# Kernel tuning notes

Hardware: AMD Instinct MI355X
Metric: run time of the kernel (lower is better)

The kernel has to match this reference:

```python
import jax, jax.numpy as jnp
import numpy as np

F_IN, F_OUT, H, L_ENC, L_DEC, HORIZON = 32, 8, 64, 2, 2, 48
B, T = 2048, 512


def _lstm_cell(x, h, c, Wih, Whh, bih, bhh):
    # PyTorch LSTMCell: gates ordered i, f, g, o
    g = x @ Wih.T + bih + h @ Whh.T + bhh
    i, f, gg, o = jnp.split(g, 4, axis=-1)
    c_new = jax.nn.sigmoid(f) * c + jax.nn.sigmoid(i) * jnp.tanh(gg)
    h_new = jax.nn.sigmoid(o) * jnp.tanh(c_new)
    return h_new, c_new


def setup_inputs() -> dict:
    key = jax.random.key(0)
    ks = jax.random.split(key, 16)
    s = 1.0 / np.sqrt(H)
    u = lambda k, shape: jax.random.uniform(k, shape, jnp.float32, -s, s)
    return {
        "X": jax.random.normal(ks[0], (B, T, F_IN), jnp.float32),
        "X_mask": jnp.ones((B, T, F_IN), jnp.float32),
        "W_emb": u(ks[1], (H, F_IN)),
        "b_emb": u(ks[2], (H,)),
        "enc_Wih": u(ks[3], (L_ENC, 4 * H, H)),
        "enc_Whh": u(ks[4], (L_ENC, 4 * H, H)),
        "enc_bih": u(ks[5], (L_ENC, 4 * H)),
        "enc_bhh": u(ks[6], (L_ENC, 4 * H)),
        "dec_Wih": u(ks[7], (L_DEC, 4 * H, H)),
        "dec_Whh": u(ks[8], (L_DEC, 4 * H, H)),
        "dec_bih": u(ks[9], (L_DEC, 4 * H)),
        "dec_bhh": u(ks[10], (L_DEC, 4 * H)),
        "W_reg": u(ks[11], (F_OUT, H)),
        "b_reg": u(ks[12], (F_OUT,)),
    }


def reference(X, X_mask, W_emb, b_emb, enc_Wih, enc_Whh, enc_bih, enc_bhh,
              dec_Wih, dec_Whh, dec_bih, dec_bhh, W_reg, b_reg):
    batch = X.shape[0]
    # Token embedding for all timesteps at once: [T, B, H]
    emb = jnp.einsum('btf,hf->tbh', X, W_emb) + b_emb

    h0 = jnp.zeros((L_ENC, batch, H), X.dtype)
    c0 = jnp.zeros((L_ENC, batch, H), X.dtype)

    def enc_step(carry, x_t):
        h, c = carry
        h_t = x_t
        hs, cs = [], []
        for i in range(L_ENC):
            h_t, c_t = _lstm_cell(h_t, h[i], c[i], enc_Wih[i], enc_Whh[i], enc_bih[i], enc_bhh[i])
            hs.append(h_t)
            cs.append(c_t)
        return (jnp.stack(hs), jnp.stack(cs)), None

    (h_enc, _), _ = jax.lax.scan(enc_step, (h0, c0), emb)

    # Decoder: hidden states initialized from encoder h, cells from zero
    c_dec0 = jnp.zeros((L_DEC, batch, H), X.dtype)

    def dec_step(carry, _):
        h, c = carry
        h_t = h[-1]
        hs, cs = [], []
        for i in range(L_DEC):
            h_t, c_t = _lstm_cell(h_t, h[i], c[i], dec_Wih[i], dec_Whh[i], dec_bih[i], dec_bhh[i])
            hs.append(h_t)
            cs.append(c_t)
        y_t = h_t @ W_reg.T + b_reg
        return (jnp.stack(hs), jnp.stack(cs)), y_t

    _, ys = jax.lax.scan(dec_step, (h_enc, c_dec0), None, length=HORIZON)
    return jnp.transpose(ys, (1, 0, 2))  # [B, horizon, F_OUT]
```

## Files before the change

kernel.cpp:

```cpp
#include <hip/hip_runtime.h>
#include <hip/hip_bf16.h>

typedef __bf16 bf16x8 __attribute__((ext_vector_type(8)));
typedef float  f32x4  __attribute__((ext_vector_type(4)));

#define MFMA16(a,b,c) __builtin_amdgcn_mfma_f32_16x16x32_bf16((a),(b),(c),0,0,0)

__device__ __forceinline__ bf16x8 cvt8(f32x4 a, f32x4 b){
  bf16x8 r;
  r[0]=(__bf16)a[0]; r[1]=(__bf16)a[1]; r[2]=(__bf16)a[2]; r[3]=(__bf16)a[3];
  r[4]=(__bf16)b[0]; r[5]=(__bf16)b[1]; r[6]=(__bf16)b[2]; r[7]=(__bf16)b[3];
  return r;
}
__device__ __forceinline__ bf16x8 ld8(const float* p){
  return cvt8(*(const f32x4*)p, *(const f32x4*)(p+4));
}
__device__ __forceinline__ float sigm(float x){
  return __builtin_amdgcn_rcpf(1.f + __expf(-x));
}
__device__ __forceinline__ float tanhx(float x){
  return 1.f - 2.f*__builtin_amdgcn_rcpf(1.f + __expf(2.f*x));
}
__device__ __forceinline__ f32x4 sp(float v){ return (f32x4){v,v,v,v}; }

extern "C" __global__ void __launch_bounds__(512, 1)
seq2seq_kernel(const float* __restrict__ X,
               const float* __restrict__ Wemb, const float* __restrict__ bemb,
               const float* __restrict__ eWih, const float* __restrict__ eWhh,
               const float* __restrict__ ebih, const float* __restrict__ ebhh,
               const float* __restrict__ dWih, const float* __restrict__ dWhh,
               const float* __restrict__ dbih, const float* __restrict__ dbhh,
               const float* __restrict__ Wreg, const float* __restrict__ breg,
               float* __restrict__ out)
{
  __shared__ __align__(16) __bf16 XA[2][8][136];
  __shared__ __align__(16) __bf16 H1s[8][72];
  __shared__ __align__(16) float  Gm[2][8][260];

  const int tid  = (int)threadIdx.x;
  const int w    = tid >> 6;
  const int grp  = w >> 2;
  const bool g0  = (grp == 0);
  const int wt   = w & 3;
  const int lane = tid & 63;
  const int col  = lane & 15;
  const int quad = lane >> 4;
  const int row8 = col & 7;
  const int b0   = (int)blockIdx.x * 8;
  const int brow = b0 + row8;

  for (int i = tid; i < 2*8*136; i += 512) (&XA[0][0][0])[i] = (__bf16)0.f;
  for (int i = tid; i < 8*72;    i += 512) (&H1s[0][0])[i]   = (__bf16)0.f;

  const int ue = wt*16 + col;
  bf16x8 wembf = ld8(Wemb + ue*32 + quad*8);
  const float eb = bemb[ue];

  bf16x8 wr[2];
#pragma unroll
  for (int ks=0; ks<2; ++ks) wr[ks] = ld8(Wreg + (col&7)*64 + ks*32 + quad*8);
  const float rb = breg[col&7];

  bf16x8 wf[16];
  float  gb[4];
#pragma unroll
  for (int j=0; j<4; ++j){
    const int n = 64*wt + 16*j + col;
    gb[j] = ebih[grp*256+n] + ebhh[grp*256+n];
#pragma unroll
    for (int ks=0; ks<4; ++ks){
      const float* srcw = (ks < 2) ? eWih : eWhh;
      wf[j*4+ks] = ld8(srcw + ((size_t)(grp*256+n))*64 + (ks&1)*32 + quad*8);
    }
  }

  float cA = 0.f, cB = 0.f;
  const float* xb = X + (size_t)brow*512*32 + quad*8;
  f32x4 pa0, pb0, pa1, pb1;
  f32x4 x0a = *(const f32x4*)xb, x0b = *(const f32x4*)(xb+4);
  pa1 = *(const f32x4*)(xb+32); pb1 = *(const f32x4*)(xb+36);
  pa0 = *(const f32x4*)(xb+64); pb0 = *(const f32x4*)(xb+68);

  auto GEMM0 = [&](const int I){
    const int Px = (I+1)&1, Pr = I&1;
    bf16x8 ax0 = *(const bf16x8*)&XA[Px][row8][ 0 + quad*8];
    bf16x8 ax1 = *(const bf16x8*)&XA[Px][row8][32 + quad*8];
    bf16x8 ah0 = *(const bf16x8*)&XA[Pr][row8][64 + quad*8];
    bf16x8 ah1 = *(const bf16x8*)&XA[Pr][row8][96 + quad*8];
    f32x4 A0=sp(gb[0]), A1=sp(gb[1]), A2=sp(gb[2]), A3=sp(gb[3]);
    A0=MFMA16(ax0,wf[0],A0);  A1=MFMA16(ax0,wf[4],A1);
    A2=MFMA16(ax0,wf[8],A2);  A3=MFMA16(ax0,wf[12],A3);
    A0=MFMA16(ax1,wf[1],A0);  A1=MFMA16(ax1,wf[5],A1);
    A2=MFMA16(ax1,wf[9],A2);  A3=MFMA16(ax1,wf[13],A3);
    A0=MFMA16(ah0,wf[2],A0);  A1=MFMA16(ah0,wf[6],A1);
    A2=MFMA16(ah0,wf[10],A2); A3=MFMA16(ah0,wf[14],A3);
    A0=MFMA16(ah1,wf[3],A0);  A1=MFMA16(ah1,wf[7],A1);
    A2=MFMA16(ah1,wf[11],A2); A3=MFMA16(ah1,wf[15],A3);
    if (I < 510){
      const int s = I&1;
      f32x4 xr0 = s ? pa1 : pa0, xr1 = s ? pb1 : pb0;
      f32x4 ea = MFMA16(cvt8(xr0,xr1), wembf, sp(eb));
      int tn = I+4; if (tn > 511) tn = 511;
      f32x4 na = *(const f32x4*)(xb + (size_t)tn*32);
      f32x4 nb = *(const f32x4*)(xb + (size_t)tn*32 + 4);
      if (s){ pa1=na; pb1=nb; } else { pa0=na; pb0=nb; }
      if (quad < 2){
#pragma unroll
        for (int r=0; r<4; ++r) XA[s][quad*4+r][ue] = (__bf16)ea[r];
      }
    }
    f32x4 t0 = (quad&2) ? A2 : A0;
    f32x4 t1 = (quad&2) ? A3 : A1;
    const int rb2 = (quad&1)*4;
    const int nn  = 64*wt + ((quad&2)?32:0) + col;
#pragma unroll
    for (int r=0; r<4; ++r){ Gm[0][rb2+r][nn] = t0[r]; Gm[0][rb2+r][nn+16] = t1[r]; }
  };

  auto GEMM1 = [&](const int I){
    const int Pr = I&1;
    bf16x8 ah0 = *(const bf16x8*)&XA[Pr][row8][64 + quad*8];
    bf16x8 ah1 = *(const bf16x8*)&XA[Pr][row8][96 + quad*8];
    bf16x8 ag0 = *(const bf16x8*)&H1s[row8][quad*8];
    bf16x8 ag1 = *(const bf16x8*)&H1s[row8][32 + quad*8];
    f32x4 A0=sp(gb[0]), A1=sp(gb[1]), A2=sp(gb[2]), A3=sp(gb[3]);
    A0=MFMA16(ah0,wf[0],A0);  A1=MFMA16(ah0,wf[4],A1);
    A2=MFMA16(ah0,wf[8],A2);  A3=MFMA16(ah0,wf[12],A3);
    A0=MFMA16(ah1,wf[1],A0);  A1=MFMA16(ah1,wf[5],A1);
    A2=MFMA16(ah1,wf[9],A2);  A3=MFMA16(ah1,wf[13],A3);
    A0=MFMA16(ag0,wf[2],A0);  A1=MFMA16(ag0,wf[6],A1);
    A2=MFMA16(ag0,wf[10],A2); A3=MFMA16(ag0,wf[14],A3);
    A0=MFMA16(ag1,wf[3],A0);  A1=MFMA16(ag1,wf[7],A1);
    A2=MFMA16(ag1,wf[11],A2); A3=MFMA16(ag1,wf[15],A3);
    f32x4 t0 = (quad&2) ? A2 : A0;
    f32x4 t1 = (quad&2) ? A3 : A1;
    const int rb2 = (quad&1)*4;
    const int nn  = 64*wt + ((quad&2)?32:0) + col;
#pragma unroll
    for (int r=0; r<4; ++r){ Gm[1][rb2+r][nn] = t0[r]; Gm[1][rb2+r][nn+16] = t1[r]; }
  };

  auto EW0 = [&](const int I){
    const int Pw = (I+1)&1;
    const float* ga = Gm[0][wt];
    const float* gc = Gm[0][wt+4];
    float iA=sigm(ga[lane]),    iB=sigm(gc[lane]);
    float fA=sigm(ga[64+lane]), fB=sigm(gc[64+lane]);
    float gA=tanhx(ga[128+lane]), gB=tanhx(gc[128+lane]);
    float oA=sigm(ga[192+lane]),  oB=sigm(gc[192+lane]);
    cA = fA*cA + iA*gA;
    cB = fB*cB + iB*gB;
    XA[Pw][wt  ][64+lane] = (__bf16)(oA*tanhx(cA));
    XA[Pw][wt+4][64+lane] = (__bf16)(oB*tanhx(cB));
  };

  auto EW1 = [&](){
    const float* ga = Gm[1][wt];
    const float* gc = Gm[1][wt+4];
    float iA=sigm(ga[lane]),    iB=sigm(gc[lane]);
    float fA=sigm(ga[64+lane]), fB=sigm(gc[64+lane]);
    float gA=tanhx(ga[128+lane]), gB=tanhx(gc[128+lane]);
    float oA=sigm(ga[192+lane]),  oB=sigm(gc[192+lane]);
    cA = fA*cA + iA*gA;
    cB = fB*cB + iB*gB;
    H1s[wt  ][lane] = (__bf16)(oA*tanhx(cA));
    H1s[wt+4][lane] = (__bf16)(oB*tanhx(cB));
  };

  __syncthreads();

  if (g0){
    f32x4 e0 = MFMA16(cvt8(x0a,x0b), wembf, sp(eb));
    if (quad < 2){
#pragma unroll
      for (int r=0; r<4; ++r) XA[0][quad*4+r][ue] = (__bf16)e0[r];
    }
  }
  __syncthreads();
  if (g0) GEMM0(-1);
  __syncthreads();
  if (g0) EW0(-1);
  __syncthreads();

#define SLOT(I)                                              \
  if (g0) GEMM0(I); else { if ((I) > 0) EW1(); }             \
  __syncthreads();                                           \
  if (g0) EW0(I); else GEMM1(I);                             \
  __syncthreads();

  for (int ii=0; ii<255; ++ii){
    SLOT(2*ii)
    SLOT(2*ii+1)
  }
  SLOT(510)
#undef SLOT

  if (!g0) EW1();
  __syncthreads();
  if (!g0) GEMM1(511);
  __syncthreads();
  if (!g0) EW1();
  __syncthreads();

  for (int idx = tid; idx < 8*128; idx += 512){
    int r = idx >> 7, cc = idx & 127;
    XA[0][r][cc] = (cc < 64) ? H1s[r][cc] : XA[1][r][cc];
  }
#pragma unroll
  for (int l=0; l<2; ++l)
#pragma unroll
    for (int ti=0; ti<2; ++ti){
      const int n = 32*w + 16*ti + col;
      gb[l*2+ti] = dbih[l*256+n] + dbhh[l*256+n];
#pragma unroll
      for (int ks=0; ks<4; ++ks){
        const float* srcw = (ks < 2) ? dWih : dWhh;
        wf[(l*2+ti)*4+ks] = ld8(srcw + ((size_t)(l*256+n))*64 + (ks&1)*32 + quad*8);
      }
    }
  float cD0 = 0.f, cD1 = 0.f;
  __syncthreads();

  auto Ystore = [&](const int t){
    f32x4 ya = sp(rb);
    bf16x8 y0 = *(const bf16x8*)&H1s[row8][quad*8];
    bf16x8 y1 = *(const bf16x8*)&H1s[row8][32 + quad*8];
    ya = MFMA16(y0, wr[0], ya);
    ya = MFMA16(y1, wr[1], ya);
    if (quad < 2 && col < 8){
#pragma unroll
      for (int r=0; r<4; ++r)
        out[((size_t)(b0 + quad*4 + r)*48 + t)*8 + col] = ya[r];
    }
  };

  for (int t=0; t<48; ++t){
    {
      bf16x8 ax0 = *(const bf16x8*)&XA[0][row8][ 0 + quad*8];
      bf16x8 ax1 = *(const bf16x8*)&XA[0][row8][32 + quad*8];
      bf16x8 ah0 = *(const bf16x8*)&XA[0][row8][64 + quad*8];
      bf16x8 ah1 = *(const bf16x8*)&XA[0][row8][96 + quad*8];
      f32x4 B0 = sp(gb[0]), B1 = sp(gb[1]);
      B0=MFMA16(ax0,wf[0],B0); B1=MFMA16(ax0,wf[4],B1);
      B0=MFMA16(ax1,wf[1],B0); B1=MFMA16(ax1,wf[5],B1);
      B0=MFMA16(ah0,wf[2],B0); B1=MFMA16(ah0,wf[6],B1);
      B0=MFMA16(ah1,wf[3],B0); B1=MFMA16(ah1,wf[7],B1);
      f32x4 t0 = (quad&2) ? B1 : B0;
      const int rb2 = (quad&1)*4, nn = 32*w + ((quad&2)?16:0) + col;
#pragma unroll
      for (int r=0; r<4; ++r) Gm[0][rb2+r][nn] = t0[r];
      if (t && w == 0) Ystore(t-1);
    }
    __syncthreads();
    {
      const float* g = Gm[0][w];
      float i0=sigm(g[lane]), f0=sigm(g[64+lane]);
      float gg=tanhx(g[128+lane]), o0=sigm(g[192+lane]);
      cD0 = f0*cD0 + i0*gg;
      XA[0][w][64+lane] = (__bf16)(o0*tanhx(cD0));
    }
    __syncthreads();
    {
      bf16x8 ah0 = *(const bf16x8*)&XA[0][row8][64 + quad*8];
      bf16x8 ah1 = *(const bf16x8*)&XA[0][row8][96 + quad*8];
      bf16x8 ag0 = *(const bf16x8*)&H1s[row8][quad*8];
      bf16x8 ag1 = *(const bf16x8*)&H1s[row8][32 + quad*8];
      f32x4 B0 = sp(gb[2]), B1 = sp(gb[3]);
      B0=MFMA16(ah0,wf[8],B0);  B1=MFMA16(ah0,wf[12],B1);
      B0=MFMA16(ah1,wf[9],B0);  B1=MFMA16(ah1,wf[13],B1);
      B0=MFMA16(ag0,wf[10],B0); B1=MFMA16(ag0,wf[14],B1);
      B0=MFMA16(ag1,wf[11],B0); B1=MFMA16(ag1,wf[15],B1);
      f32x4 t0 = (quad&2) ? B1 : B0;
      const int rb2 = (quad&1)*4, nn = 32*w + ((quad&2)?16:0) + col;
#pragma unroll
      for (int r=0; r<4; ++r) Gm[1][rb2+r][nn] = t0[r];
    }
    __syncthreads();
    {
      const float* g = Gm[1][w];
      float i1=sigm(g[lane]), f1=sigm(g[64+lane]);
      float gg=tanhx(g[128+lane]), o1=sigm(g[192+lane]);
      cD1 = f1*cD1 + i1*gg;
      __bf16 hb = (__bf16)(o1*tanhx(cD1));
      H1s[w][lane]  = hb;
      XA[0][w][lane] = hb;
    }
    __syncthreads();
  }
  if (w == 0) Ystore(47);
}

extern "C" void kernel_launch(void* const* d_in, const int* in_sizes, int n_in,
                              void* d_out, int out_size, void* d_ws, size_t ws_size,
                              hipStream_t stream)
{
  (void)in_sizes; (void)n_in; (void)out_size; (void)d_ws; (void)ws_size;
  const float* X    = (const float*)d_in[0];
  const float* Wemb = (const float*)d_in[2];
  const float* bemb = (const float*)d_in[3];
  const float* eWih = (const float*)d_in[4];
  const float* eWhh = (const float*)d_in[5];
  const float* ebih = (const float*)d_in[6];
  const float* ebhh = (const float*)d_in[7];
  const float* dWih = (const float*)d_in[8];
  const float* dWhh = (const float*)d_in[9];
  const float* dbih = (const float*)d_in[10];
  const float* dbhh = (const float*)d_in[11];
  const float* Wreg = (const float*)d_in[12];
  const float* breg = (const float*)d_in[13];
  float* out = (float*)d_out;

  seq2seq_kernel<<<dim3(256), dim3(512), 0, stream>>>(
      X, Wemb, bemb, eWih, eWhh, ebih, ebhh,
      dWih, dWhh, dbih, dbhh, Wreg, breg, out);
}
```

Before: 651.6 us.

## Double threads per block to split LSTM gate work across sixteen waves

Raises the block from 512 to 1024 threads, so each layer group has eight waves instead of four. Each wave now computes two gate tiles instead of four and runs the elementwise update for one batch row instead of two. The decoder is remapped so that waves 0-7 and 8-15 each handle one layer's elementwise step. The goal is to shorten the per-step serial critical path inside the recurrence. In exchange, barriers now cover twice as many waves, and during the decoder's elementwise phases half the waves sit idle.

After: 628.4 us. 3.5% less time.

```diff
diff --git a/kernel.cpp b/kernel.cpp
--- a/kernel.cpp
+++ b/kernel.cpp
@@ -23,7 +23,7 @@
 }
 __device__ __forceinline__ f32x4 sp(float v){ return (f32x4){v,v,v,v}; }
 
-extern "C" __global__ void __launch_bounds__(512, 1)
+extern "C" __global__ void __launch_bounds__(1024, 4)
 seq2seq_kernel(const float* __restrict__ X,
                const float* __restrict__ Wemb, const float* __restrict__ bemb,
                const float* __restrict__ eWih, const float* __restrict__ eWhh,
@@ -33,15 +33,15 @@
                const float* __restrict__ Wreg, const float* __restrict__ breg,
                float* __restrict__ out)
 {
-  __shared__ __align__(16) __bf16 XA[2][8][136];
-  __shared__ __align__(16) __bf16 H1s[8][72];
-  __shared__ __align__(16) float  Gm[2][8][260];
+  __shared__ __align__(16) __bf16 XA[2][8][144];
+  __shared__ __align__(16) __bf16 H1s[8][80];
+  __shared__ __align__(16) float  Gm[2][8][264];
 
   const int tid  = (int)threadIdx.x;
   const int w    = tid >> 6;
-  const int grp  = w >> 2;
+  const int grp  = w >> 3;
   const bool g0  = (grp == 0);
-  const int wt   = w & 3;
+  const int wt   = w & 7;
   const int lane = tid & 63;
   const int col  = lane & 15;
   const int quad = lane >> 4;
@@ -49,37 +49,35 @@
   const int b0   = (int)blockIdx.x * 8;
   const int brow = b0 + row8;
 
-  for (int i = tid; i < 2*8*136; i += 512) (&XA[0][0][0])[i] = (__bf16)0.f;
-  for (int i = tid; i < 8*72;    i += 512) (&H1s[0][0])[i]   = (__bf16)0.f;
-
-  const int ue = wt*16 + col;
-  bf16x8 wembf = ld8(Wemb + ue*32 + quad*8);
-  const float eb = bemb[ue];
-
-  bf16x8 wr[2];
-#pragma unroll
-  for (int ks=0; ks<2; ++ks) wr[ks] = ld8(Wreg + (col&7)*64 + ks*32 + quad*8);
-  const float rb = breg[col&7];
-
-  bf16x8 wf[16];
-  float  gb[4];
-#pragma unroll
-  for (int j=0; j<4; ++j){
-    const int n = 64*wt + 16*j + col;
-    gb[j] = ebih[grp*256+n] + ebhh[grp*256+n];
+  for (int i = tid; i < 2*8*144; i += 1024) (&XA[0][0][0])[i] = (__bf16)0.f;
+  for (int i = tid; i < 8*80;    i += 1024) (&H1s[0][0])[i]   = (__bf16)0.f;
+
+  bf16x8 wf[8];
+  float  gb[2];
+#pragma unroll
+  for (int ti=0; ti<2; ++ti){
+    const int n = 32*wt + 16*ti + col;
+    gb[ti] = ebih[grp*256+n] + ebhh[grp*256+n];
 #pragma unroll
     for (int ks=0; ks<4; ++ks){
       const float* srcw = (ks < 2) ? eWih : eWhh;
-      wf[j*4+ks] = ld8(srcw + ((size_t)(grp*256+n))*64 + (ks&1)*32 + quad*8);
-    }
-  }
-
-  float cA = 0.f, cB = 0.f;
+      wf[ti*4+ks] = ld8(srcw + ((size_t)(grp*256+n))*64 + (ks&1)*32 + quad*8);
+    }
+  }
+
+  const int ue = (w&3)*16 + col;
+  bf16x8 wembf;
+  float eb = 0.f;
   const float* xb = X + (size_t)brow*512*32 + quad*8;
   f32x4 pa0, pb0, pa1, pb1;
-  f32x4 x0a = *(const f32x4*)xb, x0b = *(const f32x4*)(xb+4);
-  pa1 = *(const f32x4*)(xb+32); pb1 = *(const f32x4*)(xb+36);
-  pa0 = *(const f32x4*)(xb+64); pb0 = *(const f32x4*)(xb+68);
+  if (w < 4){
+    wembf = ld8(Wemb + ue*32 + quad*8);
+    eb = bemb[ue];
+    pa1 = *(const f32x4*)(xb+32); pb1 = *(const f32x4*)(xb+36);
+    pa0 = *(const f32x4*)(xb+64); pb0 = *(const f32x4*)(xb+68);
+  }
+
+  float cC = 0.f;
 
   auto GEMM0 = [&](const int I){
     const int Px = (I+1)&1, Pr = I&1;
@@ -87,16 +85,12 @@
     bf16x8 ax1 = *(const bf16x8*)&XA[Px][row8][32 + quad*8];
     bf16x8 ah0 = *(const bf16x8*)&XA[Pr][row8][64 + quad*8];
     bf16x8 ah1 = *(const bf16x8*)&XA[Pr][row8][96 + quad*8];
-    f32x4 A0=sp(gb[0]), A1=sp(gb[1]), A2=sp(gb[2]), A3=sp(gb[3]);
-    A0=MFMA16(ax0,wf[0],A0);  A1=MFMA16(ax0,wf[4],A1);
-    A2=MFMA16(ax0,wf[8],A2);  A3=MFMA16(ax0,wf[12],A3);
-    A0=MFMA16(ax1,wf[1],A0);  A1=MFMA16(ax1,wf[5],A1);
-    A2=MFMA16(ax1,wf[9],A2);  A3=MFMA16(ax1,wf[13],A3);
-    A0=MFMA16(ah0,wf[2],A0);  A1=MFMA16(ah0,wf[6],A1);
-    A2=MFMA16(ah0,wf[10],A2); A3=MFMA16(ah0,wf[14],A3);
-    A0=MFMA16(ah1,wf[3],A0);  A1=MFMA16(ah1,wf[7],A1);
-    A2=MFMA16(ah1,wf[11],A2); A3=MFMA16(ah1,wf[15],A3);
-    if (I < 510){
+    f32x4 A0 = sp(gb[0]), A1 = sp(gb[1]);
+    A0=MFMA16(ax0,wf[0],A0); A1=MFMA16(ax0,wf[4],A1);
+    A0=MFMA16(ax1,wf[1],A0); A1=MFMA16(ax1,wf[5],A1);
+    A0=MFMA16(ah0,wf[2],A0); A1=MFMA16(ah0,wf[6],A1);
+    A0=MFMA16(ah1,wf[3],A0); A1=MFMA16(ah1,wf[7],A1);
+    if (I < 510 && w < 4){
       const int s = I&1;
       f32x4 xr0 = s ? pa1 : pa0, xr1 = s ? pb1 : pb0;
       f32x4 ea = MFMA16(cvt8(xr0,xr1), wembf, sp(eb));
@@ -109,12 +103,11 @@
         for (int r=0; r<4; ++r) XA[s][quad*4+r][ue] = (__bf16)ea[r];
       }
     }
-    f32x4 t0 = (quad&2) ? A2 : A0;
-    f32x4 t1 = (quad&2) ? A3 : A1;
+    f32x4 t0 = (quad&2) ? A1 : A0;
     const int rb2 = (quad&1)*4;
-    const int nn  = 64*wt + ((quad&2)?32:0) + col;
-#pragma unroll
-    for (int r=0; r<4; ++r){ Gm[0][rb2+r][nn] = t0[r]; Gm[0][rb2+r][nn+16] = t1[r]; }
+    const int nn  = 32*wt + ((quad&2)?16:0) + col;
+#pragma unroll
+    for (int r=0; r<4; ++r) Gm[0][rb2+r][nn] = t0[r];
   };
 
   auto GEMM1 = [&](const int I){
@@ -123,53 +116,39 @@
     bf16x8 ah1 = *(const bf16x8*)&XA[Pr][row8][96 + quad*8];
     bf16x8 ag0 = *(const bf16x8*)&H1s[row8][quad*8];
     bf16x8 ag1 = *(const bf16x8*)&H1s[row8][32 + quad*8];
-    f32x4 A0=sp(gb[0]), A1=sp(gb[1]), A2=sp(gb[2]), A3=sp(gb[3]);
-    A0=MFMA16(ah0,wf[0],A0);  A1=MFMA16(ah0,wf[4],A1);
-    A2=MFMA16(ah0,wf[8],A2);  A3=MFMA16(ah0,wf[12],A3);
-    A0=MFMA16(ah1,wf[1],A0);  A1=MFMA16(ah1,wf[5],A1);
-    A2=MFMA16(ah1,wf[9],A2);  A3=MFMA16(ah1,wf[13],A3);
-    A0=MFMA16(ag0,wf[2],A0);  A1=MFMA16(ag0,wf[6],A1);
-    A2=MFMA16(ag0,wf[10],A2); A3=MFMA16(ag0,wf[14],A3);
-    A0=MFMA16(ag1,wf[3],A0);  A1=MFMA16(ag1,wf[7],A1);
-    A2=MFMA16(ag1,wf[11],A2); A3=MFMA16(ag1,wf[15],A3);
-    f32x4 t0 = (quad&2) ? A2 : A0;
-    f32x4 t1 = (quad&2) ? A3 : A1;
+    f32x4 A0 = sp(gb[0]), A1 = sp(gb[1]);
+    A0=MFMA16(ah0,wf[0],A0); A1=MFMA16(ah0,wf[4],A1);
+    A0=MFMA16(ah1,wf[1],A0); A1=MFMA16(ah1,wf[5],A1);
+    A0=MFMA16(ag0,wf[2],A0); A1=MFMA16(ag0,wf[6],A1);
+    A0=MFMA16(ag1,wf[3],A0); A1=MFMA16(ag1,wf[7],A1);
+    f32x4 t0 = (quad&2) ? A1 : A0;
     const int rb2 = (quad&1)*4;
-    const int nn  = 64*wt + ((quad&2)?32:0) + col;
-#pragma unroll
-    for (int r=0; r<4; ++r){ Gm[1][rb2+r][nn] = t0[r]; Gm[1][rb2+r][nn+16] = t1[r]; }
+    const int nn  = 32*wt + ((quad&2)?16:0) + col;
+#pragma unroll
+    for (int r=0; r<4; ++r) Gm[1][rb2+r][nn] = t0[r];
   };
 
   auto EW0 = [&](const int I){
     const int Pw = (I+1)&1;
-    const float* ga = Gm[0][wt];
-    const float* gc = Gm[0][wt+4];
-    float iA=sigm(ga[lane]),    iB=sigm(gc[lane]);
-    float fA=sigm(ga[64+lane]), fB=sigm(gc[64+lane]);
-    float gA=tanhx(ga[128+lane]), gB=tanhx(gc[128+lane]);
-    float oA=sigm(ga[192+lane]),  oB=sigm(gc[192+lane]);
-    cA = fA*cA + iA*gA;
-    cB = fB*cB + iB*gB;
-    XA[Pw][wt  ][64+lane] = (__bf16)(oA*tanhx(cA));
-    XA[Pw][wt+4][64+lane] = (__bf16)(oB*tanhx(cB));
+    const float* g = Gm[0][wt];
+    float i0=sigm(g[lane]),      f0=sigm(g[64+lane]);
+    float gg=tanhx(g[128+lane]), o0=sigm(g[192+lane]);
+    cC = f0*cC + i0*gg;
+    XA[Pw][wt][64+lane] = (__bf16)(o0*tanhx(cC));
   };
 
   auto EW1 = [&](){
-    const float* ga = Gm[1][wt];
-    const float* gc = Gm[1][wt+4];
-    float iA=sigm(ga[lane]),    iB=sigm(gc[lane]);
-    float fA=sigm(ga[64+lane]), fB=sigm(gc[64+lane]);
-    float gA=tanhx(ga[128+lane]), gB=tanhx(gc[128+lane]);
-    float oA=sigm(ga[192+lane]),  oB=sigm(gc[192+lane]);
-    cA = fA*cA + iA*gA;
-    cB = fB*cB + iB*gB;
-    H1s[wt  ][lane] = (__bf16)(oA*tanhx(cA));
-    H1s[wt+4][lane] = (__bf16)(oB*tanhx(cB));
-  };
-
-  __syncthreads();
-
-  if (g0){
+    const float* g = Gm[1][wt];
+    float i1=sigm(g[lane]),      f1=sigm(g[64+lane]);
+    float gg=tanhx(g[128+lane]), o1=sigm(g[192+lane]);
+    cC = f1*cC + i1*gg;
+    H1s[wt][lane] = (__bf16)(o1*tanhx(cC));
+  };
+
+  __syncthreads();
+
+  if (w < 4){
+    f32x4 x0a = *(const f32x4*)xb, x0b = *(const f32x4*)(xb+4);
     f32x4 e0 = MFMA16(cvt8(x0a,x0b), wembf, sp(eb));
     if (quad < 2){
 #pragma unroll
@@ -202,31 +181,33 @@
   if (!g0) EW1();
   __syncthreads();
 
-  for (int idx = tid; idx < 8*128; idx += 512){
+  for (int idx = tid; idx < 8*128; idx += 1024){
     int r = idx >> 7, cc = idx & 127;
     XA[0][r][cc] = (cc < 64) ? H1s[r][cc] : XA[1][r][cc];
   }
-#pragma unroll
-  for (int l=0; l<2; ++l)
-#pragma unroll
-    for (int ti=0; ti<2; ++ti){
-      const int n = 32*w + 16*ti + col;
-      gb[l*2+ti] = dbih[l*256+n] + dbhh[l*256+n];
-#pragma unroll
-      for (int ks=0; ks<4; ++ks){
-        const float* srcw = (ks < 2) ? dWih : dWhh;
-        wf[(l*2+ti)*4+ks] = ld8(srcw + ((size_t)(l*256+n))*64 + (ks&1)*32 + quad*8);
-      }
-    }
-  float cD0 = 0.f, cD1 = 0.f;
+  bf16x8 wr0 = ld8(Wreg + (col&7)*64 +  0 + quad*8);
+  bf16x8 wr1 = ld8(Wreg + (col&7)*64 + 32 + quad*8);
+  const float rb = breg[col&7];
+  float gbd[2];
+#pragma unroll
+  for (int l=0; l<2; ++l){
+    const int n = 16*w + col;
+    gbd[l] = dbih[l*256+n] + dbhh[l*256+n];
+#pragma unroll
+    for (int ks=0; ks<4; ++ks){
+      const float* srcw = (ks < 2) ? dWih : dWhh;
+      wf[l*4+ks] = ld8(srcw + ((size_t)(l*256+n))*64 + (ks&1)*32 + quad*8);
+    }
+  }
+  cC = 0.f;
   __syncthreads();
 
   auto Ystore = [&](const int t){
     f32x4 ya = sp(rb);
     bf16x8 y0 = *(const bf16x8*)&H1s[row8][quad*8];
     bf16x8 y1 = *(const bf16x8*)&H1s[row8][32 + quad*8];
-    ya = MFMA16(y0, wr[0], ya);
-    ya = MFMA16(y1, wr[1], ya);
+    ya = MFMA16(y0, wr0, ya);
+    ya = MFMA16(y1, wr1, ya);
     if (quad < 2 && col < 8){
 #pragma unroll
       for (int r=0; r<4; ++r)
@@ -240,24 +221,24 @@
       bf16x8 ax1 = *(const bf16x8*)&XA[0][row8][32 + quad*8];
       bf16x8 ah0 = *(const bf16x8*)&XA[0][row8][64 + quad*8];
       bf16x8 ah1 = *(const bf16x8*)&XA[0][row8][96 + quad*8];
-      f32x4 B0 = sp(gb[0]), B1 = sp(gb[1]);
-      B0=MFMA16(ax0,wf[0],B0); B1=MFMA16(ax0,wf[4],B1);
-      B0=MFMA16(ax1,wf[1],B0); B1=MFMA16(ax1,wf[5],B1);
-      B0=MFMA16(ah0,wf[2],B0); B1=MFMA16(ah0,wf[6],B1);
-      B0=MFMA16(ah1,wf[3],B0); B1=MFMA16(ah1,wf[7],B1);
-      f32x4 t0 = (quad&2) ? B1 : B0;
-      const int rb2 = (quad&1)*4, nn = 32*w + ((quad&2)?16:0) + col;
-#pragma unroll
-      for (int r=0; r<4; ++r) Gm[0][rb2+r][nn] = t0[r];
+      f32x4 B0 = sp(gbd[0]);
+      B0=MFMA16(ax0,wf[0],B0);
+      B0=MFMA16(ax1,wf[1],B0);
+      B0=MFMA16(ah0,wf[2],B0);
+      B0=MFMA16(ah1,wf[3],B0);
+      if (quad < 2){
+#pragma unroll
+        for (int r=0; r<4; ++r) Gm[0][quad*4+r][16*w+col] = B0[r];
+      }
       if (t && w == 0) Ystore(t-1);
     }
     __syncthreads();
-    {
+    if (w < 8){
       const float* g = Gm[0][w];
-      float i0=sigm(g[lane]), f0=sigm(g[64+lane]);
+      float i0=sigm(g[lane]),      f0=sigm(g[64+lane]);
       float gg=tanhx(g[128+lane]), o0=sigm(g[192+lane]);
-      cD0 = f0*cD0 + i0*gg;
-      XA[0][w][64+lane] = (__bf16)(o0*tanhx(cD0));
+      cC = f0*cC + i0*gg;
+      XA[0][w][64+lane] = (__bf16)(o0*tanhx(cC));
     }
     __syncthreads();
     {
@@ -265,25 +246,26 @@
       bf16x8 ah1 = *(const bf16x8*)&XA[0][row8][96 + quad*8];
       bf16x8 ag0 = *(const bf16x8*)&H1s[row8][quad*8];
       bf16x8 ag1 = *(const bf16x8*)&H1s[row8][32 + quad*8];
-      f32x4 B0 = sp(gb[2]), B1 = sp(gb[3]);
-      B0=MFMA16(ah0,wf[8],B0);  B1=MFMA16(ah0,wf[12],B1);
-      B0=MFMA16(ah1,wf[9],B0);  B1=MFMA16(ah1,wf[13],B1);
-      B0=MFMA16(ag0,wf[10],B0); B1=MFMA16(ag0,wf[14],B1);
-      B0=MFMA16(ag1,wf[11],B0); B1=MFMA16(ag1,wf[15],B1);
-      f32x4 t0 = (quad&2) ? B1 : B0;
-      const int rb2 = (quad&1)*4, nn = 32*w + ((quad&2)?16:0) + col;
-#pragma unroll
-      for (int r=0; r<4; ++r) Gm[1][rb2+r][nn] = t0[r];
-    }
-    __syncthreads();
-    {
-      const float* g = Gm[1][w];
-      float i1=sigm(g[lane]), f1=sigm(g[64+lane]);
+      f32x4 B1 = sp(gbd[1]);
+      B1=MFMA16(ah0,wf[4],B1);
+      B1=MFMA16(ah1,wf[5],B1);
+      B1=MFMA16(ag0,wf[6],B1);
+      B1=MFMA16(ag1,wf[7],B1);
+      if (quad < 2){
+#pragma unroll
+        for (int r=0; r<4; ++r) Gm[1][quad*4+r][16*w+col] = B1[r];
+      }
+    }
+    __syncthreads();
+    if (w >= 8){
+      const int rw = w - 8;
+      const float* g = Gm[1][rw];
+      float i1=sigm(g[lane]),      f1=sigm(g[64+lane]);
       float gg=tanhx(g[128+lane]), o1=sigm(g[192+lane]);
-      cD1 = f1*cD1 + i1*gg;
-      __bf16 hb = (__bf16)(o1*tanhx(cD1));
-      H1s[w][lane]  = hb;
-      XA[0][w][lane] = hb;
+      cC = f1*cC + i1*gg;
+      __bf16 hb = (__bf16)(o1*tanhx(cC));
+      H1s[rw][lane]   = hb;
+      XA[0][rw][lane] = hb;
     }
     __syncthreads();
   }
@@ -310,7 +292,7 @@
   const float* breg = (const float*)d_in[13];
   float* out = (float*)d_out;
 
-  seq2seq_kernel<<<dim3(256), dim3(512), 0, stream>>>(
+  seq2seq_kernel<<<dim3(256), dim3(1024), 0, stream>>>(
       X, Wemb, bemb, eWih, eWhh, ebih, ebhh,
       dWih, dWhh, dbih, dbhh, Wreg, breg, out);
 }
```

## Halve batch rows per block to launch twice as many blocks

Applied to the files above, without the earlier changes.

Each block now handles 4 batch rows instead of 8, and the grid doubles from 256 to 512 blocks. Launch bounds are relaxed to allow multiple blocks per CU. The elementwise and gate-store mappings are rearranged so each wave handles one row, and in the decoder the two layers' elementwise work is split between the wave halves. The aim is to fill more CUs, since the strictly serial time recurrence leaves the machine underused. The trade-off is that the 16-row MFMA tiles are now only a quarter used, so more matrix instructions are wasted per useful row.

New measurement: 1.660 ms. 155% more time.

```diff
diff --git a/kernel.cpp b/kernel.cpp
--- a/kernel.cpp
+++ b/kernel.cpp
@@ -23,7 +23,7 @@
 }
 __device__ __forceinline__ f32x4 sp(float v){ return (f32x4){v,v,v,v}; }
 
-extern "C" __global__ void __launch_bounds__(512, 1)
+extern "C" __global__ void __launch_bounds__(512, 4)
 seq2seq_kernel(const float* __restrict__ X,
                const float* __restrict__ Wemb, const float* __restrict__ bemb,
                const float* __restrict__ eWih, const float* __restrict__ eWhh,
@@ -33,33 +33,24 @@
                const float* __restrict__ Wreg, const float* __restrict__ breg,
                float* __restrict__ out)
 {
-  __shared__ __align__(16) __bf16 XA[2][8][136];
-  __shared__ __align__(16) __bf16 H1s[8][72];
-  __shared__ __align__(16) float  Gm[2][8][260];
+  __shared__ __align__(16) __bf16 XA[2][4][144];
+  __shared__ __align__(16) __bf16 H1s[4][80];
+  __shared__ __align__(16) float  Gm[2][4][264];
 
   const int tid  = (int)threadIdx.x;
   const int w    = tid >> 6;
+  const bool g0  = (w < 4);
   const int grp  = w >> 2;
-  const bool g0  = (grp == 0);
   const int wt   = w & 3;
   const int lane = tid & 63;
   const int col  = lane & 15;
   const int quad = lane >> 4;
-  const int row8 = col & 7;
-  const int b0   = (int)blockIdx.x * 8;
-  const int brow = b0 + row8;
-
-  for (int i = tid; i < 2*8*136; i += 512) (&XA[0][0][0])[i] = (__bf16)0.f;
-  for (int i = tid; i < 8*72;    i += 512) (&H1s[0][0])[i]   = (__bf16)0.f;
-
-  const int ue = wt*16 + col;
-  bf16x8 wembf = ld8(Wemb + ue*32 + quad*8);
-  const float eb = bemb[ue];
-
-  bf16x8 wr[2];
-#pragma unroll
-  for (int ks=0; ks<2; ++ks) wr[ks] = ld8(Wreg + (col&7)*64 + ks*32 + quad*8);
-  const float rb = breg[col&7];
+  const int row4 = col & 3;
+  const int b0   = (int)blockIdx.x * 4;
+  const int brow = b0 + row4;
+
+  for (int i = tid; i < 2*4*144; i += 512) (&XA[0][0][0])[i] = (__bf16)0.f;
+  for (int i = tid; i < 4*80;    i += 512) (&H1s[0][0])[i]   = (__bf16)0.f;
 
   bf16x8 wf[16];
   float  gb[4];
@@ -74,19 +65,26 @@
     }
   }
 
-  float cA = 0.f, cB = 0.f;
+  const int ue = wt*16 + col;
+  bf16x8 wembf;
+  float eb = 0.f;
   const float* xb = X + (size_t)brow*512*32 + quad*8;
   f32x4 pa0, pb0, pa1, pb1;
-  f32x4 x0a = *(const f32x4*)xb, x0b = *(const f32x4*)(xb+4);
-  pa1 = *(const f32x4*)(xb+32); pb1 = *(const f32x4*)(xb+36);
-  pa0 = *(const f32x4*)(xb+64); pb0 = *(const f32x4*)(xb+68);
+  if (g0){
+    wembf = ld8(Wemb + ue*32 + quad*8);
+    eb = bemb[ue];
+    pa1 = *(const f32x4*)(xb+32); pb1 = *(const f32x4*)(xb+36);
+    pa0 = *(const f32x4*)(xb+64); pb0 = *(const f32x4*)(xb+68);
+  }
+
+  float cC = 0.f;
 
   auto GEMM0 = [&](const int I){
     const int Px = (I+1)&1, Pr = I&1;
-    bf16x8 ax0 = *(const bf16x8*)&XA[Px][row8][ 0 + quad*8];
-    bf16x8 ax1 = *(const bf16x8*)&XA[Px][row8][32 + quad*8];
-    bf16x8 ah0 = *(const bf16x8*)&XA[Pr][row8][64 + quad*8];
-    bf16x8 ah1 = *(const bf16x8*)&XA[Pr][row8][96 + quad*8];
+    bf16x8 ax0 = *(const bf16x8*)&XA[Px][row4][ 0 + quad*8];
+    bf16x8 ax1 = *(const bf16x8*)&XA[Px][row4][32 + quad*8];
+    bf16x8 ah0 = *(const bf16x8*)&XA[Pr][row4][64 + quad*8];
+    bf16x8 ah1 = *(const bf16x8*)&XA[Pr][row4][96 + quad*8];
     f32x4 A0=sp(gb[0]), A1=sp(gb[1]), A2=sp(gb[2]), A3=sp(gb[3]);
     A0=MFMA16(ax0,wf[0],A0);  A1=MFMA16(ax0,wf[4],A1);
     A2=MFMA16(ax0,wf[8],A2);  A3=MFMA16(ax0,wf[12],A3);
@@ -104,25 +102,25 @@
       f32x4 na = *(const f32x4*)(xb + (size_t)tn*32);
       f32x4 nb = *(const f32x4*)(xb + (size_t)tn*32 + 4);
       if (s){ pa1=na; pb1=nb; } else { pa0=na; pb0=nb; }
-      if (quad < 2){
-#pragma unroll
-        for (int r=0; r<4; ++r) XA[s][quad*4+r][ue] = (__bf16)ea[r];
+      if (quad == 0){
+#pragma unroll
+        for (int r=0; r<4; ++r) XA[s][r][ue] = (__bf16)ea[r];
       }
     }
-    f32x4 t0 = (quad&2) ? A2 : A0;
-    f32x4 t1 = (quad&2) ? A3 : A1;
-    const int rb2 = (quad&1)*4;
-    const int nn  = 64*wt + ((quad&2)?32:0) + col;
-#pragma unroll
-    for (int r=0; r<4; ++r){ Gm[0][rb2+r][nn] = t0[r]; Gm[0][rb2+r][nn+16] = t1[r]; }
+    f32x4 u0 = (quad&1) ? A1 : A0;
+    f32x4 u1 = (quad&1) ? A3 : A2;
+    f32x4 t  = (quad&2) ? u1 : u0;
+    const int nn = 64*wt + 16*quad + col;
+#pragma unroll
+    for (int r=0; r<4; ++r) Gm[0][r][nn] = t[r];
   };
 
   auto GEMM1 = [&](const int I){
     const int Pr = I&1;
-    bf16x8 ah0 = *(const bf16x8*)&XA[Pr][row8][64 + quad*8];
-    bf16x8 ah1 = *(const bf16x8*)&XA[Pr][row8][96 + quad*8];
-    bf16x8 ag0 = *(const bf16x8*)&H1s[row8][quad*8];
-    bf16x8 ag1 = *(const bf16x8*)&H1s[row8][32 + quad*8];
+    bf16x8 ah0 = *(const bf16x8*)&XA[Pr][row4][64 + quad*8];
+    bf16x8 ah1 = *(const bf16x8*)&XA[Pr][row4][96 + quad*8];
+    bf16x8 ag0 = *(const bf16x8*)&H1s[row4][quad*8];
+    bf16x8 ag1 = *(const bf16x8*)&H1s[row4][32 + quad*8];
     f32x4 A0=sp(gb[0]), A1=sp(gb[1]), A2=sp(gb[2]), A3=sp(gb[3]);
     A0=MFMA16(ah0,wf[0],A0);  A1=MFMA16(ah0,wf[4],A1);
     A2=MFMA16(ah0,wf[8],A2);  A3=MFMA16(ah0,wf[12],A3);
@@ -132,48 +130,39 @@
     A2=MFMA16(ag0,wf[10],A2); A3=MFMA16(ag0,wf[14],A3);
     A0=MFMA16(ag1,wf[3],A0);  A1=MFMA16(ag1,wf[7],A1);
     A2=MFMA16(ag1,wf[11],A2); A3=MFMA16(ag1,wf[15],A3);
-    f32x4 t0 = (quad&2) ? A2 : A0;
-    f32x4 t1 = (quad&2) ? A3 : A1;
-    const int rb2 = (quad&1)*4;
-    const int nn  = 64*wt + ((quad&2)?32:0) + col;
-#pragma unroll
-    for (int r=0; r<4; ++r){ Gm[1][rb2+r][nn] = t0[r]; Gm[1][rb2+r][nn+16] = t1[r]; }
+    f32x4 u0 = (quad&1) ? A1 : A0;
+    f32x4 u1 = (quad&1) ? A3 : A2;
+    f32x4 t  = (quad&2) ? u1 : u0;
+    const int nn = 64*wt + 16*quad + col;
+#pragma unroll
+    for (int r=0; r<4; ++r) Gm[1][r][nn] = t[r];
   };
 
   auto EW0 = [&](const int I){
     const int Pw = (I+1)&1;
-    const float* ga = Gm[0][wt];
-    const float* gc = Gm[0][wt+4];
-    float iA=sigm(ga[lane]),    iB=sigm(gc[lane]);
-    float fA=sigm(ga[64+lane]), fB=sigm(gc[64+lane]);
-    float gA=tanhx(ga[128+lane]), gB=tanhx(gc[128+lane]);
-    float oA=sigm(ga[192+lane]),  oB=sigm(gc[192+lane]);
-    cA = fA*cA + iA*gA;
-    cB = fB*cB + iB*gB;
-    XA[Pw][wt  ][64+lane] = (__bf16)(oA*tanhx(cA));
-    XA[Pw][wt+4][64+lane] = (__bf16)(oB*tanhx(cB));
+    const float* g = Gm[0][wt];
+    float i0=sigm(g[lane]),      f0=sigm(g[64+lane]);
+    float gg=tanhx(g[128+lane]), o0=sigm(g[192+lane]);
+    cC = f0*cC + i0*gg;
+    XA[Pw][wt][64+lane] = (__bf16)(o0*tanhx(cC));
   };
 
   auto EW1 = [&](){
-    const float* ga = Gm[1][wt];
-    const float* gc = Gm[1][wt+4];
-    float iA=sigm(ga[lane]),    iB=sigm(gc[lane]);
-    float fA=sigm(ga[64+lane]), fB=sigm(gc[64+lane]);
-    float gA=tanhx(ga[128+lane]), gB=tanhx(gc[128+lane]);
-    float oA=sigm(ga[192+lane]),  oB=sigm(gc[192+lane]);
-    cA = fA*cA + iA*gA;
-    cB = fB*cB + iB*gB;
-    H1s[wt  ][lane] = (__bf16)(oA*tanhx(cA));
-    H1s[wt+4][lane] = (__bf16)(oB*tanhx(cB));
+    const float* g = Gm[1][wt];
+    float i1=sigm(g[lane]),      f1=sigm(g[64+lane]);
+    float gg=tanhx(g[128+lane]), o1=sigm(g[192+lane]);
+    cC = f1*cC + i1*gg;
+    H1s[wt][lane] = (__bf16)(o1*tanhx(cC));
   };
 
   __syncthreads();
 
   if (g0){
+    f32x4 x0a = *(const f32x4*)xb, x0b = *(const f32x4*)(xb+4);
     f32x4 e0 = MFMA16(cvt8(x0a,x0b), wembf, sp(eb));
-    if (quad < 2){
-#pragma unroll
-      for (int r=0; r<4; ++r) XA[0][quad*4+r][ue] = (__bf16)e0[r];
+    if (quad == 0){
+#pragma unroll
+      for (int r=0; r<4; ++r) XA[0][r][ue] = (__bf16)e0[r];
     }
   }
   __syncthreads();
@@ -202,10 +191,13 @@
   if (!g0) EW1();
   __syncthreads();
 
-  for (int idx = tid; idx < 8*128; idx += 512){
+  for (int idx = tid; idx < 4*128; idx += 512){
     int r = idx >> 7, cc = idx & 127;
     XA[0][r][cc] = (cc < 64) ? H1s[r][cc] : XA[1][r][cc];
   }
+  bf16x8 wr0 = ld8(Wreg + (col&7)*64 +  0 + quad*8);
+  bf16x8 wr1 = ld8(Wreg + (col&7)*64 + 32 + quad*8);
+  const float rb = breg[col&7];
 #pragma unroll
   for (int l=0; l<2; ++l)
 #pragma unroll
@@ -218,72 +210,77 @@
         wf[(l*2+ti)*4+ks] = ld8(srcw + ((size_t)(l*256+n))*64 + (ks&1)*32 + quad*8);
       }
     }
-  float cD0 = 0.f, cD1 = 0.f;
+  cC = 0.f;
   __syncthreads();
 
   auto Ystore = [&](const int t){
     f32x4 ya = sp(rb);
-    bf16x8 y0 = *(const bf16x8*)&H1s[row8][quad*8];
-    bf16x8 y1 = *(const bf16x8*)&H1s[row8][32 + quad*8];
-    ya = MFMA16(y0, wr[0], ya);
-    ya = MFMA16(y1, wr[1], ya);
-    if (quad < 2 && col < 8){
+    bf16x8 y0 = *(const bf16x8*)&H1s[row4][quad*8];
+    bf16x8 y1 = *(const bf16x8*)&H1s[row4][32 + quad*8];
+    ya = MFMA16(y0, wr0, ya);
+    ya = MFMA16(y1, wr1, ya);
+    if (quad == 0 && col < 8){
 #pragma unroll
       for (int r=0; r<4; ++r)
-        out[((size_t)(b0 + quad*4 + r)*48 + t)*8 + col] = ya[r];
+        out[((size_t)(b0 + r)*48 + t)*8 + col] = ya[r];
     }
   };
 
   for (int t=0; t<48; ++t){
     {
-      bf16x8 ax0 = *(const bf16x8*)&XA[0][row8][ 0 + quad*8];
-      bf16x8 ax1 = *(const bf16x8*)&XA[0][row8][32 + quad*8];
-      bf16x8 ah0 = *(const bf16x8*)&XA[0][row8][64 + quad*8];
-      bf16x8 ah1 = *(const bf16x8*)&XA[0][row8][96 + quad*8];
+      bf16x8 ax0 = *(const bf16x8*)&XA[0][row4][ 0 + quad*8];
+      bf16x8 ax1 = *(const bf16x8*)&XA[0][row4][32 + quad*8];
+      bf16x8 ah0 = *(const bf16x8*)&XA[0][row4][64 + quad*8];
+      bf16x8 ah1 = *(const bf16x8*)&XA[0][row4][96 + quad*8];
       f32x4 B0 = sp(gb[0]), B1 = sp(gb[1]);
       B0=MFMA16(ax0,wf[0],B0); B1=MFMA16(ax0,wf[4],B1);
       B0=MFMA16(ax1,wf[1],B0); B1=MFMA16(ax1,wf[5],B1);
       B0=MFMA16(ah0,wf[2],B0); B1=MFMA16(ah0,wf[6],B1);
       B0=MFMA16(ah1,wf[3],B0); B1=MFMA16(ah1,wf[7],B1);
-      f32x4 t0 = (quad&2) ? B1 : B0;
-      const int rb2 = (quad&1)*4, nn = 32*w + ((quad&2)?16:0) + col;
-#pragma unroll
-      for (int r=0; r<4; ++r) Gm[0][rb2+r][nn] = t0[r];
+      if (quad < 2){
+        f32x4 t0 = (quad&1) ? B1 : B0;
+        const int nn = 32*w + ((quad&1)?16:0) + col;
+#pragma unroll
+        for (int r=0; r<4; ++r) Gm[0][r][nn] = t0[r];
+      }
       if (t && w == 0) Ystore(t-1);
+    }
+    __syncthreads();
+    if (w < 4){
+      const float* g = Gm[0][w];
+      float i0=sigm(g[lane]),      f0=sigm(g[64+lane]);
+      float gg=tanhx(g[128+lane]), o0=sigm(g[192+lane]);
+      cC = f0*cC + i0*gg;
+      XA[0][w][64+lane] = (__bf16)(o0*tanhx(cC));
     }
     __syncthreads();
     {
-      const float* g = Gm[0][w];
-      float i0=sigm(g[lane]), f0=sigm(g[64+lane]);
-      float gg=tanhx(g[128+lane]), o0=sigm(g[192+lane]);
-      cD0 = f0*cD0 + i0*gg;
-      XA[0][w][64+lane] = (__bf16)(o0*tanhx(cD0));
-    }
-    __syncthreads();
-    {
-      bf16x8 ah0 = *(const bf16x8*)&XA[0][row8][64 + quad*8];
-      bf16x8 ah1 = *(const bf16x8*)&XA[0][row8][96 + quad*8];
-      bf16x8 ag0 = *(const bf16x8*)&H1s[row8][quad*8];
-      bf16x8 ag1 = *(const bf16x8*)&H1s[row8][32 + quad*8];
+      bf16x8 ah0 = *(const bf16x8*)&XA[0][row4][64 + quad*8];
+      bf16x8 ah1 = *(const bf16x8*)&XA[0][row4][96 + quad*8];
+      bf16x8 ag0 = *(const bf16x8*)&H1s[row4][quad*8];
+      bf16x8 ag1 = *(const bf16x8*)&H1s[row4][32 + quad*8];
       f32x4 B0 = sp(gb[2]), B1 = sp(gb[3]);
       B0=MFMA16(ah0,wf[8],B0);  B1=MFMA16(ah0,wf[12],B1);
       B0=MFMA16(ah1,wf[9],B0);  B1=MFMA16(ah1,wf[13],B1);
       B0=MFMA16(ag0,wf[10],B0); B1=MFMA16(ag0,wf[14],B1);
       B0=MFMA16(ag1,wf[11],B0); B1=MFMA16(ag1,wf[15],B1);
-      f32x4 t0 = (quad&2) ? B1 : B0;
-      const int rb2 = (quad&1)*4, nn = 32*w + ((quad&2)?16:0) + col;
-#pragma unroll
-      for (int r=0; r<4; ++r) Gm[1][rb2+r][nn] = t0[r];
+      if (quad < 2){
+        f32x4 t0 = (quad&1) ? B1 : B0;
+        const int nn = 32*w + ((quad&1)?16:0) + col;
+#pragma unroll
+        for (int r=0; r<4; ++r) Gm[1][r][nn] = t0[r];
+      }
     }
     __syncthreads();
-    {
-      const float* g = Gm[1][w];
-      float i1=sigm(g[lane]), f1=sigm(g[64+lane]);
+    if (w >= 4){
+      const int rw = w - 4;
+      const float* g = Gm[1][rw];
+      float i1=sigm(g[lane]),      f1=sigm(g[64+lane]);
       float gg=tanhx(g[128+lane]), o1=sigm(g[192+lane]);
-      cD1 = f1*cD1 + i1*gg;
-      __bf16 hb = (__bf16)(o1*tanhx(cD1));
-      H1s[w][lane]  = hb;
-      XA[0][w][lane] = hb;
+      cC = f1*cC + i1*gg;
+      __bf16 hb = (__bf16)(o1*tanhx(cC));
+      H1s[rw][lane]   = hb;
+      XA[0][rw][lane] = hb;
     }
     __syncthreads();
   }
@@ -310,7 +307,7 @@
   const float* breg = (const float*)d_in[13];
   float* out = (float*)d_out;
 
-  seq2seq_kernel<<<dim3(256), dim3(512), 0, stream>>>(
+  seq2seq_kernel<<<dim3(512), dim3(512), 0, stream>>>(
       X, Wemb, bemb, eWih, eWhh, ebih, ebhh,
       dWih, dWhh, dbih, dbhh, Wreg, breg, out);
 }
```
